# Kernel optimization log

Hardware: AMD Instinct MI355X
Metric: run time of the kernel (lower is better)

The kernel has to match this reference:

```python
import jax, jax.numpy as jnp
import numpy as np

C = 1.0          # curvature magnitude (args.c)
K = C            # geoopt Lorentz k parameter
EPS = 1e-15
NUM_LAYERS = 3   # resSumGCN propagation depth
CLAMP1 = 50.0    # dist2 clamp for id embeddings
CLAMP2 = 15.0    # dist2 clamp for tag embeddings

# ---- Lorentz manifold math (geoopt conventions, <x,x>_L = -K) ----

def projx(x):
    # project onto hyperboloid: x0 = sqrt(K + ||x_rest||^2)
    x0 = jnp.sqrt(K + jnp.sum(x[..., 1:] ** 2, axis=-1, keepdims=True))
    return jnp.concatenate([x0, x[..., 1:]], axis=-1)

def expmap0(u_rest):
    # exp map at origin; u_rest is the spatial part of the tangent vector
    sk = jnp.sqrt(K)
    norm = jnp.sqrt(jnp.clip(jnp.sum(u_rest ** 2, axis=-1, keepdims=True), EPS))
    x0 = sk * jnp.cosh(norm / sk)
    xr = sk * jnp.sinh(norm / sk) * u_rest / norm
    return jnp.concatenate([x0, xr], axis=-1)

def logmap0(x):
    # log map at origin; returns spatial part of tangent vector
    sk = jnp.sqrt(K)
    alpha = jnp.clip(x[..., :1] / sk, 1.0 + 1e-7)
    rest = x[..., 1:]
    rnorm = jnp.sqrt(jnp.clip(jnp.sum(rest ** 2, axis=-1, keepdims=True), EPS))
    return sk * jnp.arccosh(alpha) * rest / rnorm

def dist2(x, y):
    # squared geodesic distance, keepdim=True -> [..., 1]
    inner = -x[..., :1] * y[..., :1] + jnp.sum(x[..., 1:] * y[..., 1:], axis=-1, keepdims=True)
    d = jnp.clip(-inner / K, 1.0 + 1e-7)
    a = jnp.arccosh(d)
    return K * a * a

def l2p(x):
    # lorentz -> poincare: drops the time coordinate
    return x[..., 1:] / (x[..., :1] + jnp.sqrt(K))

def p2l(x):
    # poincare -> lorentz: adds the time coordinate
    nx = jnp.sum(x ** 2, axis=-1, keepdims=True)
    sk = jnp.sqrt(K)
    num = jnp.concatenate([K + nx, 2.0 * sk * x], axis=-1)
    return sk * num / (K - nx + 1e-6)

def p2k(x):
    denom = 1.0 + C * jnp.sum(x ** 2, axis=-1, keepdims=True)
    return 2.0 * x / denom

def k2p(x):
    denom = 1.0 + jnp.sqrt(jnp.clip(1.0 - C * jnp.sum(x ** 2, axis=-1, keepdims=True), EPS))
    return x / denom

def lorentz_factor(x):
    return 1.0 / jnp.sqrt(jnp.clip(1.0 - C * jnp.sum(x ** 2, axis=-1, keepdims=True), EPS))

def hyper_agg(weights, x):
    # Lorentz-factor weighted Einstein midpoint aggregation
    x_k = p2k(l2p(x))                                   # klein coords [T, d]
    gamma = lorentz_factor(jax.lax.stop_gradient(x_k))  # [T, 1] (detached)
    num = weights @ (gamma * x_k)                        # [M, d]
    den = jnp.clip(weights @ gamma, EPS)                 # [M, 1]
    return p2l(k2p(num / den))                           # [M, d+1]

def encoder_encode(x, edge_src, edge_dst, edge_weight, n_nodes):
    # HGCF-style resSumGCN: tangent-space propagation, sum of powers 1..L
    xt = logmap0(x)
    cur = xt
    acc = jnp.zeros_like(xt)
    for _ in range(NUM_LAYERS):
        msg = edge_weight[:, None] * cur[edge_src]       # [E, d]
        cur = jax.ops.segment_sum(msg, edge_dst, num_segments=n_nodes)
        acc = acc + cur
    return expmap0(acc)


def setup_inputs() -> dict:
    key = jax.random.key(0)
    ks = jax.random.split(key, 8)
    N_USERS, N_ITEMS, D, TAGS = 8192, 40960, 64, 1024
    N = N_USERS + N_ITEMS
    E, B = 1572864, 131072
    emb_weight = 0.1 * jax.random.normal(ks[0], (N, D), dtype=jnp.float32)
    T_weight = 0.1 * jax.random.normal(ks[1], (TAGS, D), dtype=jnp.float32)
    ugr_weight = 0.1 * jax.random.normal(ks[2], (N_USERS, D), dtype=jnp.float32)
    sps = jax.random.uniform(ks[3], (N_ITEMS, TAGS), dtype=jnp.float32)
    sps = sps / jnp.sum(sps, axis=1, keepdims=True)      # row-normalized tag matrix
    edge_src = jax.random.randint(ks[4], (E,), 0, N)
    edge_dst = jax.random.randint(ks[5], (E,), 0, N)
    edge_weight = jax.random.uniform(ks[6], (E,), dtype=jnp.float32) / 32.0
    u = jax.random.randint(ks[7], (B,), 0, N_USERS)
    i = jax.random.randint(jax.random.fold_in(key, 99), (B,), N_USERS, N)
    idx = jnp.stack([u, i], axis=1)
    return {"emb_weight": emb_weight, "T_weight": T_weight, "ugr_weight": ugr_weight,
            "sps": sps, "edge_weight": edge_weight, "edge_src": edge_src,
            "edge_dst": edge_dst, "idx": idx}


def reference(emb_weight, T_weight, ugr_weight, sps, edge_weight, edge_src, edge_dst, idx):
    N, D = emb_weight.shape
    # ---- encode ----
    x1 = projx(emb_weight)
    h_in = encoder_encode(x1, edge_src, edge_dst, edge_weight, N)   # [N, D]
    emb_tag = projx(T_weight)
    emb_tag_in = projx(ugr_weight)                                  # users
    emb_tag_out = hyper_agg(sps, emb_tag)                           # items [N_items, D]
    x2 = jnp.concatenate([emb_tag_in, emb_tag_out], axis=0)         # [N, D]
    h_gr = encoder_encode(x2, edge_src, edge_dst, edge_weight, N)   # [N, D]
    h = jnp.concatenate([h_in, h_gr], axis=-1)                      # [N, 2D]
    # ---- decode ----
    emb_in = h[idx[:, 0], :D]
    emb_out = h[idx[:, 1], :D]
    sq = jnp.minimum(dist2(emb_in, emb_out), CLAMP1)
    tag_in = h[idx[:, 0], D:]
    tag_out = h[idx[:, 1], D:]
    sq = sq + jnp.minimum(dist2(tag_in, tag_out), CLAMP2)
    return sq  # [B, 1]
```

## Files before the change

### kernel.cpp

```cpp
#include <hip/hip_runtime.h>


#define KSPLIT 2
#define NBUK 96
#define CAP 18432

__device__ __forceinline__ float wsum(float v) {
#pragma unroll
  for (int m = 32; m; m >>= 1) v += __shfl_xor(v, m, 64);
  return v;
}

__device__ __forceinline__ float logmap_scale(float ss) {
  float x0 = sqrtf(1.0f + ss);
  float alpha = fmaxf(x0, 1.0f + 1e-7f);
  float rnorm = sqrtf(fmaxf(ss, 1e-15f));
  return acoshf(alpha) / rnorm;
}


__device__ void passA_body(
    const int* __restrict__ esrc, const int* __restrict__ edst,
    const float* __restrict__ ew, int* __restrict__ bcur,
    int2* __restrict__ stage, int bx) {
  __shared__ int lh[128];
  __shared__ int lscan[128];
  __shared__ int lcur[128];
  __shared__ int gb[128];
  __shared__ unsigned int keyb[2048];
  __shared__ float wvb[2048];
  int tid = threadIdx.x;
  int base = bx * 2048;
  if (tid < 128) lh[tid] = 0;
  __syncthreads();
  unsigned int key[8]; float wv[8];
#pragma unroll
  for (int r = 0; r < 8; ++r) {
    int e = base + r * 256 + tid;
    int d = edst[e];
    key[r] = ((unsigned int)d << 16) | (unsigned int)esrc[e];
    wv[r] = ew[e];
    atomicAdd(&lh[d >> 9], 1);
  }
  __syncthreads();
  if (tid < 128) lscan[tid] = lh[tid];
  __syncthreads();
  for (int d = 1; d < 128; d <<= 1) {
    int v = (tid < 128 && tid >= d) ? lscan[tid - d] : 0;
    __syncthreads();
    if (tid < 128) lscan[tid] += v;
    __syncthreads();
  }
  if (tid < 128) {
    int excl = lscan[tid] - lh[tid];
    lscan[tid] = excl;
    lcur[tid] = 0;
    if (tid < NBUK && lh[tid] > 0) {
      int rsv = atomicAdd(&bcur[tid], lh[tid]);
      gb[tid] = tid * CAP + rsv;
    }
  }
  __syncthreads();
#pragma unroll
  for (int r = 0; r < 8; ++r) {
    int b = key[r] >> 25;
    int lp = lscan[b] + atomicAdd(&lcur[b], 1);
    keyb[lp] = key[r];
    wvb[lp] = wv[r];
  }
  __syncthreads();
#pragma unroll
  for (int r = 0; r < 8; ++r) {
    int i = r * 256 + tid;
    unsigned int k2 = keyb[i];
    int b = k2 >> 25;
    stage[gb[b] + (i - lscan[b])] = make_int2((int)k2, __float_as_int(wvb[i]));
  }
}

__device__ void prep_body(
    const float* __restrict__ emb, const float* __restrict__ ugr,
    const float* __restrict__ Tw, float* __restrict__ xt,
    float* __restrict__ gkg, int N, int NU, int TAGS, int pbx) {
  int n = pbx * 4 + (threadIdx.x >> 6);
  int lane = threadIdx.x & 63;
  if (n < N) {
    size_t base = (size_t)n * 128;
    float r1 = (lane < 63) ? emb[(size_t)n * 64 + 1 + lane] : 0.0f;
    float sc1 = logmap_scale(wsum(r1 * r1));
    if (lane < 63) xt[base + lane] = sc1 * r1;
    if (lane == 63) { xt[base + 126] = 0.0f; xt[base + 127] = 0.0f; }
    if (n < NU) {
      float r2 = (lane < 63) ? ugr[(size_t)n * 64 + 1 + lane] : 0.0f;
      float sc2 = logmap_scale(wsum(r2 * r2));
      if (lane < 63) xt[base + 63 + lane] = sc2 * r2;
    }
  } else if (n < N + TAGS) {
    int t = n - N;
    float r = (lane < 63) ? Tw[(size_t)t * 64 + 1 + lane] : 0.0f;
    float ss = wsum(r * r);
    float x0 = sqrtf(1.0f + ss);
    float p = r / (x0 + 1.0f);
    float sp = wsum(p * p);
    float k = 2.0f * p / (1.0f + sp);
    float sk2 = wsum(k * k);
    float gamma = 1.0f / sqrtf(fmaxf(1.0f - sk2, 1e-15f));
    gkg[(size_t)t * 64 + lane] = (lane < 63) ? gamma * k : gamma;
  }
}

__global__ __launch_bounds__(256) void k_mega1(
    const int* __restrict__ esrc, const int* __restrict__ edst,
    const float* __restrict__ ew, int* __restrict__ bcur,
    int2* __restrict__ stage,
    const float* __restrict__ emb, const float* __restrict__ ugr,
    const float* __restrict__ Tw, float* __restrict__ xt,
    float* __restrict__ gkg, int N, int NU, int TAGS, int nA) {
  if ((int)blockIdx.x < nA)
    passA_body(esrc, edst, ew, bcur, stage, blockIdx.x);
  else
    prep_body(emb, ugr, Tw, xt, gkg, N, NU, TAGS, blockIdx.x - nA);
}


__device__ void passB2_body(
    const int2* __restrict__ stage, const int* __restrict__ bcur,
    int* __restrict__ off, int2* __restrict__ rec, int N, int E) {
  __shared__ int hist[512];
  __shared__ int pairs[256];
  __shared__ int cur[512];
  __shared__ int bs[128];
  int b = blockIdx.x, tid = threadIdx.x;
  if (tid < 128) bs[tid] = (tid < NBUK) ? min(bcur[tid], CAP) : 0;
  hist[tid] = 0; hist[tid + 256] = 0;
  __syncthreads();
  for (int d = 1; d < 128; d <<= 1) {
    int v = (tid < 128 && tid >= d) ? bs[tid - d] : 0;
    __syncthreads();
    if (tid < 128) bs[tid] += v;
    __syncthreads();
  }
  int cnt = min(bcur[b], CAP);
  int base = bs[b] - cnt;
  if (b == 0 && tid == 0) off[N] = E;
  const int2* sg = stage + (size_t)b * CAP;
  for (int i = tid; i < cnt; i += 256)
    atomicAdd(&hist[((unsigned int)sg[i].x >> 16) & 511], 1);
  __syncthreads();
  int h0 = hist[2 * tid], h1 = hist[2 * tid + 1];
  int ps = h0 + h1;
  pairs[tid] = ps;
  __syncthreads();
  for (int d = 1; d < 256; d <<= 1) {
    int v = (tid >= d) ? pairs[tid - d] : 0;
    __syncthreads();
    pairs[tid] += v;
    __syncthreads();
  }
  int e0 = base + pairs[tid] - ps;
  int e1 = e0 + h0;
  int gd = b * 512 + 2 * tid;
  off[gd] = e0;      cur[2 * tid] = e0;
  off[gd + 1] = e1;  cur[2 * tid + 1] = e1;
  __syncthreads();
  for (int i = tid; i < cnt; i += 256) {
    int2 r = sg[i];
    unsigned int k2 = (unsigned int)r.x;
    int d = (int)((k2 >> 16) & 511);
    int p = atomicAdd(&cur[d], 1);
    rec[p] = make_int2((int)(k2 & 0xFFFF), r.y);
  }
}

__device__ void hyper_body(
    const float* __restrict__ sps, const float* __restrict__ gkg,
    float* __restrict__ pb, int NI, int bx, int ksp) {
  __shared__ float g_tile[32 * 64];
  int tid = threadIdx.x;
  int tx = tid & 15, ty = tid >> 4;
  int gx = tid & 15, gy = tid >> 4;
  int ib = bx * 64;
  int kbase = ksp * (1024 / KSPLIT);
  float acc[4][4];
#pragma unroll
  for (int c = 0; c < 4; ++c)
#pragma unroll
    for (int d = 0; d < 4; ++d) acc[c][d] = 0.0f;

  const float4* sps4 = (const float4*)sps;
  const float4* gkg4 = (const float4*)gkg;
  size_t rb[4];
#pragma unroll
  for (int c = 0; c < 4; ++c) rb[c] = (size_t)(ib + ty * 4 + c) * 256;

  for (int kc = 0; kc < (1024 / KSPLIT) / 32; ++kc) {
#pragma unroll
    for (int r = 0; r < 2; ++r) {
      int grow = gy + 16 * r;
      *(float4*)&g_tile[grow * 64 + gx * 4] =
          gkg4[(size_t)(kbase + kc * 32 + grow) * 16 + gx];
    }
    __syncthreads();
    int t4 = (kbase >> 2) + kc * 8;
    float4 A[4], Nb[4];
#pragma unroll
    for (int c = 0; c < 4; ++c) A[c] = sps4[rb[c] + t4];
#pragma unroll
    for (int tg = 0; tg < 8; ++tg) {
#pragma unroll
      for (int c = 0; c < 4; ++c)
        if (tg < 7) Nb[c] = sps4[rb[c] + t4 + tg + 1];
      float4 g4[4];
#pragma unroll
      for (int j = 0; j < 4; ++j)
        g4[j] = *(const float4*)&g_tile[(tg * 4 + j) * 64 + tx * 4];
#pragma unroll
      for (int c = 0; c < 4; ++c) {
        float sv[4] = {A[c].x, A[c].y, A[c].z, A[c].w};
#pragma unroll
        for (int j = 0; j < 4; ++j) {
          acc[c][0] = fmaf(sv[j], g4[j].x, acc[c][0]);
          acc[c][1] = fmaf(sv[j], g4[j].y, acc[c][1]);
          acc[c][2] = fmaf(sv[j], g4[j].z, acc[c][2]);
          acc[c][3] = fmaf(sv[j], g4[j].w, acc[c][3]);
        }
      }
#pragma unroll
      for (int c = 0; c < 4; ++c)
        if (tg < 7) A[c] = Nb[c];
    }
    __syncthreads();
  }

  float* dst = pb + ((size_t)ksp * NI + ib) * 64;
#pragma unroll
  for (int c = 0; c < 4; ++c)
    *(float4*)&dst[(size_t)(ty * 4 + c) * 64 + tx * 4] =
        make_float4(acc[c][0], acc[c][1], acc[c][2], acc[c][3]);
}

__global__ __launch_bounds__(256) void k_mega2(
    const int2* __restrict__ stage, const int* __restrict__ bcur,
    int* __restrict__ off, int2* __restrict__ rec,
    const float* __restrict__ sps, const float* __restrict__ gkg,
    float* __restrict__ pb, int NI, int N, int E) {
  if ((int)blockIdx.x < NBUK) {
    passB2_body(stage, bcur, off, rec, N, E);
  } else {
    int hb = blockIdx.x - NBUK;
    int nbx = NI / 64;
    hyper_body(sps, gkg, pb, NI, hb % nbx, hb / nbx);
  }
}

__global__ __launch_bounds__(256) void k_combine(
    const float* __restrict__ pb, float* __restrict__ xt, int NI, int NU) {
  int i = blockIdx.x * 4 + (threadIdx.x >> 6);
  if (i >= NI) return;
  int lane = threadIdx.x & 63;
  float v = 0.0f;
#pragma unroll
  for (int s = 0; s < KSPLIT; ++s) v += pb[((size_t)s * NI + i) * 64 + lane];
  float den = fmaxf(__shfl(v, 63, 64), 1e-15f);
  float y = v / den;
  float sy = wsum((lane < 63) ? y * y : 0.0f);
  float dk = 1.0f + sqrtf(fmaxf(1.0f - sy, 1e-15f));
  float q = y / dk;
  float nq = wsum((lane < 63) ? q * q : 0.0f);
  float f = 1.0f / (1.0f - nq + 1e-6f);
  float row0 = (1.0f + nq) * f;
  float r = 2.0f * q * f;
  float srr = wsum((lane < 63) ? r * r : 0.0f);
  float alpha = fmaxf(row0, 1.0f + 1e-7f);
  float scale = acoshf(alpha) / sqrtf(fmaxf(srr, 1e-15f));
  if (lane < 63)
    xt[(size_t)(NU + i) * 128 + 63 + lane] = scale * r;
}

__device__ __forceinline__ float4 gather_row(
    const float* __restrict__ cur, const int* __restrict__ off,
    const int2* __restrict__ rec, int n, int lane) {
  int half = lane >> 5;
  int q = lane & 31;
  const float4* cq = (const float4*)cur + q;
  int beg = off[n], end = off[n + 1];
  float4 acc = make_float4(0.0f, 0.0f, 0.0f, 0.0f);
  for (int j = beg; j < end; j += 64) {
    int cnt = min(64, end - j);
    int sv = 0; float wv = 0.0f;
    if (lane < cnt) {
      int2 rc = rec[j + lane];
      sv = rc.x;
      wv = __int_as_float(rc.y);
    }
    int k = 0;
    for (; k + 16 <= cnt; k += 16) {
      int s[8]; float w[8]; float4 v[8];
#pragma unroll
      for (int u = 0; u < 8; ++u) {
        int e = k + 2 * u + half;
        s[u] = __shfl(sv, e, 64);
        w[u] = __shfl(wv, e, 64);
      }
#pragma unroll
      for (int u = 0; u < 8; ++u) v[u] = cq[(size_t)s[u] * 32];
#pragma unroll
      for (int u = 0; u < 8; ++u) {
        acc.x = fmaf(w[u], v[u].x, acc.x);
        acc.y = fmaf(w[u], v[u].y, acc.y);
        acc.z = fmaf(w[u], v[u].z, acc.z);
        acc.w = fmaf(w[u], v[u].w, acc.w);
      }
    }
    for (; k + 8 <= cnt; k += 8) {
      int s[4]; float w[4]; float4 v[4];
#pragma unroll
      for (int u = 0; u < 4; ++u) {
        int e = k + 2 * u + half;
        s[u] = __shfl(sv, e, 64);
        w[u] = __shfl(wv, e, 64);
      }
#pragma unroll
      for (int u = 0; u < 4; ++u) v[u] = cq[(size_t)s[u] * 32];
#pragma unroll
      for (int u = 0; u < 4; ++u) {
        acc.x = fmaf(w[u], v[u].x, acc.x);
        acc.y = fmaf(w[u], v[u].y, acc.y);
        acc.z = fmaf(w[u], v[u].z, acc.z);
        acc.w = fmaf(w[u], v[u].w, acc.w);
      }
    }
    for (; k + 2 <= cnt; k += 2) {
      int e = k + half;
      int s0 = __shfl(sv, e, 64);
      float w0 = __shfl(wv, e, 64);
      float4 v = cq[(size_t)s0 * 32];
      acc.x = fmaf(w0, v.x, acc.x);
      acc.y = fmaf(w0, v.y, acc.y);
      acc.z = fmaf(w0, v.z, acc.z);
      acc.w = fmaf(w0, v.w, acc.w);
    }
    if (k < cnt) {
      int s0 = __shfl(sv, k, 64);
      float w0 = __shfl(wv, k, 64);
      if (half == 0) {
        float4 v = cq[(size_t)s0 * 32];
        acc.x = fmaf(w0, v.x, acc.x);
        acc.y = fmaf(w0, v.y, acc.y);
        acc.z = fmaf(w0, v.z, acc.z);
        acc.w = fmaf(w0, v.w, acc.w);
      }
    }
  }
  acc.x += __shfl_xor(acc.x, 32, 64);
  acc.y += __shfl_xor(acc.y, 32, 64);
  acc.z += __shfl_xor(acc.z, 32, 64);
  acc.w += __shfl_xor(acc.w, 32, 64);
  return acc;
}

__global__ __launch_bounds__(256) void k_gather(
    const float* __restrict__ cur, float* __restrict__ nxt,
    const int* __restrict__ off, const int2* __restrict__ rec, int N) {
  int n = blockIdx.x * 4 + (threadIdx.x >> 6);
  if (n >= N) return;
  int lane = threadIdx.x & 63;
  float4 acc = gather_row(cur, off, rec, n, lane);
  if (lane < 32) ((float4*)(nxt + (size_t)n * 128))[lane] = acc;
}

__global__ __launch_bounds__(256) void k_gather_exp(
    const float* __restrict__ cur, const float* b1, const float* __restrict__ b2,
    const int* __restrict__ off, const int2* __restrict__ rec,
    float* h, int N) {
  int n = blockIdx.x * 4 + (threadIdx.x >> 6);
  if (n >= N) return;
  int lane = threadIdx.x & 63;
  int q = lane & 31;
  float4 a3 = gather_row(cur, off, rec, n, lane);
  size_t b = (size_t)n * 128;
  float4 r1 = ((const float4*)(b1 + b))[q];
  float4 r2 = ((const float4*)(b2 + b))[q];
  float vv[4] = {a3.x + r1.x + r2.x, a3.y + r1.y + r2.y,
                 a3.z + r1.z + r2.z, a3.w + r1.w + r2.w};
  float p0 = 0.0f, p1 = 0.0f;
#pragma unroll
  for (int i = 0; i < 4; ++i) {
    int c = 4 * q + i;
    if (c < 63) p0 += vv[i] * vv[i]; else p1 += vv[i] * vv[i];
  }
  float ss0 = 0.5f * wsum(p0);
  float ss1 = 0.5f * wsum(p1);
  float nn0 = sqrtf(fmaxf(ss0, 1e-15f)), nn1 = sqrtf(fmaxf(ss1, 1e-15f));
  float s0 = sinhf(nn0) / nn0, s1 = sinhf(nn1) / nn1;
  int prev = (lane == 0) ? 0 : lane - 1;
  float pv2 = __shfl(vv[2], prev, 64);
  float pv3 = __shfl(vv[3], prev, 64);
  if (lane < 32) {
    float4 o;
    if (q < 16) {
      o.x = (q == 0) ? coshf(nn0) : s0 * pv3;
      o.y = s0 * vv[0]; o.z = s0 * vv[1]; o.w = s0 * vv[2];
    } else {
      o.x = (q == 16) ? coshf(nn1) : s1 * pv2;
      o.y = s1 * pv3; o.z = s1 * vv[0]; o.w = s1 * vv[1];
    }
    ((float4*)(h + b))[q] = o;
  }
}

__global__ __launch_bounds__(256) void k_score(
    const float* __restrict__ h, const int* __restrict__ idx,
    float* __restrict__ out, int B) {
  int w = blockIdx.x * 4 + (threadIdx.x >> 6);
  int lane = threadIdx.x & 63;
  int b0 = w * 4;
  if (b0 >= B) return;
  int np = min(4, B - b0);
  float2 hu[4], hv[4];
#pragma unroll
  for (int p = 0; p < 4; ++p) {
    int bb = b0 + ((p < np) ? p : 0);
    int u = idx[2 * bb], v = idx[2 * bb + 1];
    hu[p] = ((const float2*)(h + (size_t)u * 128))[lane];
    hv[p] = ((const float2*)(h + (size_t)v * 128))[lane];
  }
#pragma unroll
  for (int p = 0; p < 4; ++p) {
    if (p >= np) break;
    float px = hu[p].x * hv[p].x;
    if (lane == 0 || lane == 32) px = -px;
    float pp = px + hu[p].y * hv[p].y;
#pragma unroll
    for (int m = 1; m < 32; m <<= 1) pp += __shfl_xor(pp, m, 64);
    float dd = fmaxf(-pp, 1.0f + 1e-7f);
    float a = acoshf(dd);
    float s = fminf(a * a, (lane < 32) ? 50.0f : 15.0f);
    s += __shfl_xor(s, 32, 64);
    if (lane == 0) out[b0 + p] = s;
  }
}

extern "C" void kernel_launch(void* const* d_in, const int* in_sizes, int n_in,
                              void* d_out, int out_size, void* d_ws, size_t ws_size,
                              hipStream_t stream) {
  const float* emb = (const float*)d_in[0];
  const float* Tw  = (const float*)d_in[1];
  const float* ugr = (const float*)d_in[2];
  const float* sps = (const float*)d_in[3];
  const float* ew  = (const float*)d_in[4];
  const int* esrc  = (const int*)d_in[5];
  const int* edst  = (const int*)d_in[6];
  const int* idx   = (const int*)d_in[7];
  float* out = (float*)d_out;

  const int N    = in_sizes[0] / 64;
  const int TAGS = in_sizes[1] / 64;
  const int NU   = in_sizes[2] / 64;
  const int NI   = in_sizes[3] / TAGS;
  const int E    = in_sizes[4];
  const int B    = in_sizes[7] / 2;

  size_t rowsz = (size_t)N * 128 * sizeof(float);
  char* ws = (char*)d_ws;
  float* xt  = (float*)(ws);
  float* b1  = (float*)(ws + rowsz);
  float* b2  = (float*)(ws + 2 * rowsz);
  float* gkg = (float*)(ws + 3 * rowsz);
  size_t o = 3 * rowsz + (size_t)TAGS * 64 * sizeof(float);
  int* off   = (int*)(ws + o);  o += (size_t)(N + 1) * sizeof(int);
  int* bcur  = (int*)(ws + o);  o += (size_t)NBUK * sizeof(int);
  o = (o + 7) & ~(size_t)7;
  int2* rec = (int2*)(ws + o);
  int2* stage = (int2*)b2;
  float* pb = b1;
  float* h  = b1;

  const int nA = E / 2048;
  const int nPrep = (N + TAGS + 3) / 4;
  const int nHyper = (NI / 64) * KSPLIT;

  hipMemsetAsync(bcur, 0, (size_t)NBUK * sizeof(int), stream);
  k_mega1<<<nA + nPrep, 256, 0, stream>>>(esrc, edst, ew, bcur, stage,
                                          emb, ugr, Tw, xt, gkg, N, NU, TAGS, nA);
  k_mega2<<<NBUK + nHyper, 256, 0, stream>>>(stage, bcur, off, rec,
                                             sps, gkg, pb, NI, N, E);
  k_combine<<<(NI + 3) / 4, 256, 0, stream>>>(pb, xt, NI, NU);

  k_gather<<<(N + 3) / 4, 256, 0, stream>>>(xt, b1, off, rec, N);
  k_gather<<<(N + 3) / 4, 256, 0, stream>>>(b1, b2, off, rec, N);
  k_gather_exp<<<(N + 3) / 4, 256, 0, stream>>>(b2, b1, b2, off, rec, h, N);

  k_score<<<(B / 4 + 3) / 4, 256, 0, stream>>>(h, idx, out, B);
}
```

Baseline: 545.2 us.

## Split fused pass-B/hyper kernel and retile hyper GEMM with shared-memory sps tile

Splits the combined bucket-sort pass and hyperbolic aggregation GEMM back into two separate kernel launches. The GEMM now stages a 128x32 tile of the sparse-weight matrix in padded shared memory, where before each thread streamed its rows straight from global memory. Each thread computes an 8x4 output block instead of 4x4, and KSPLIT goes from 2 to 4, with the grid laid out as a 2D (rows, k-split) grid. The aim is better reuse and coalescing of sps loads, at the cost of losing overlap between the two passes and doing more partial-sum work in combine.

```diff
diff --git a/kernel.cpp b/kernel.cpp
--- a/kernel.cpp
+++ b/kernel.cpp
@@ -1,7 +1,7 @@
 #include <hip/hip_runtime.h>
 
 
-#define KSPLIT 2
+#define KSPLIT 4
 #define NBUK 96
 #define CAP 18432
 
@@ -123,7 +123,7 @@
 }
 
 
-__device__ void passB2_body(
+__global__ __launch_bounds__(256) void k_passB2(
     const int2* __restrict__ stage, const int* __restrict__ bcur,
     int* __restrict__ off, int2* __restrict__ rec, int N, int E) {
   __shared__ int hist[512];
@@ -172,51 +172,50 @@
   }
 }
 
-__device__ void hyper_body(
+__global__ __launch_bounds__(256) void k_hyper(
     const float* __restrict__ sps, const float* __restrict__ gkg,
-    float* __restrict__ pb, int NI, int bx, int ksp) {
-  __shared__ float g_tile[32 * 64];
+    float* __restrict__ pb, int NI) {
+  __shared__ float s_tile[128][36];
+  __shared__ float g_tile[32][64];
   int tid = threadIdx.x;
   int tx = tid & 15, ty = tid >> 4;
+  int sx = tid & 7,  sy = tid >> 3;
   int gx = tid & 15, gy = tid >> 4;
-  int ib = bx * 64;
-  int kbase = ksp * (1024 / KSPLIT);
-  float acc[4][4];
-#pragma unroll
-  for (int c = 0; c < 4; ++c)
+  int ib = blockIdx.x * 128;
+  int kbase = blockIdx.y * 256;
+  float acc[8][4];
+#pragma unroll
+  for (int c = 0; c < 8; ++c)
 #pragma unroll
     for (int d = 0; d < 4; ++d) acc[c][d] = 0.0f;
 
   const float4* sps4 = (const float4*)sps;
   const float4* gkg4 = (const float4*)gkg;
-  size_t rb[4];
-#pragma unroll
-  for (int c = 0; c < 4; ++c) rb[c] = (size_t)(ib + ty * 4 + c) * 256;
-
-  for (int kc = 0; kc < (1024 / KSPLIT) / 32; ++kc) {
+
+  for (int kc = 0; kc < 8; ++kc) {
+    int t4b = (kbase >> 2) + kc * 8;
+#pragma unroll
+    for (int r = 0; r < 4; ++r) {
+      int row = sy + 32 * r;
+      *(float4*)&s_tile[row][sx * 4] = sps4[(size_t)(ib + row) * 256 + t4b + sx];
+    }
 #pragma unroll
     for (int r = 0; r < 2; ++r) {
       int grow = gy + 16 * r;
-      *(float4*)&g_tile[grow * 64 + gx * 4] =
+      *(float4*)&g_tile[grow][gx * 4] =
           gkg4[(size_t)(kbase + kc * 32 + grow) * 16 + gx];
     }
     __syncthreads();
-    int t4 = (kbase >> 2) + kc * 8;
-    float4 A[4], Nb[4];
-#pragma unroll
-    for (int c = 0; c < 4; ++c) A[c] = sps4[rb[c] + t4];
 #pragma unroll
     for (int tg = 0; tg < 8; ++tg) {
-#pragma unroll
-      for (int c = 0; c < 4; ++c)
-        if (tg < 7) Nb[c] = sps4[rb[c] + t4 + tg + 1];
       float4 g4[4];
 #pragma unroll
       for (int j = 0; j < 4; ++j)
-        g4[j] = *(const float4*)&g_tile[(tg * 4 + j) * 64 + tx * 4];
-#pragma unroll
-      for (int c = 0; c < 4; ++c) {
-        float sv[4] = {A[c].x, A[c].y, A[c].z, A[c].w};
+        g4[j] = *(const float4*)&g_tile[tg * 4 + j][tx * 4];
+#pragma unroll
+      for (int c = 0; c < 8; ++c) {
+        float4 s4 = *(const float4*)&s_tile[ty + 16 * c][tg * 4];
+        float sv[4] = {s4.x, s4.y, s4.z, s4.w};
 #pragma unroll
         for (int j = 0; j < 4; ++j) {
           acc[c][0] = fmaf(sv[j], g4[j].x, acc[c][0]);
@@ -225,32 +224,15 @@
           acc[c][3] = fmaf(sv[j], g4[j].w, acc[c][3]);
         }
       }
-#pragma unroll
-      for (int c = 0; c < 4; ++c)
-        if (tg < 7) A[c] = Nb[c];
-    }
-    __syncthreads();
-  }
-
-  float* dst = pb + ((size_t)ksp * NI + ib) * 64;
-#pragma unroll
-  for (int c = 0; c < 4; ++c)
-    *(float4*)&dst[(size_t)(ty * 4 + c) * 64 + tx * 4] =
+    }
+    __syncthreads();
+  }
+
+  float* dst = pb + ((size_t)blockIdx.y * NI + ib) * 64;
+#pragma unroll
+  for (int c = 0; c < 8; ++c)
+    *(float4*)&dst[(size_t)(ty + 16 * c) * 64 + tx * 4] =
         make_float4(acc[c][0], acc[c][1], acc[c][2], acc[c][3]);
-}
-
-__global__ __launch_bounds__(256) void k_mega2(
-    const int2* __restrict__ stage, const int* __restrict__ bcur,
-    int* __restrict__ off, int2* __restrict__ rec,
-    const float* __restrict__ sps, const float* __restrict__ gkg,
-    float* __restrict__ pb, int NI, int N, int E) {
-  if ((int)blockIdx.x < NBUK) {
-    passB2_body(stage, bcur, off, rec, N, E);
-  } else {
-    int hb = blockIdx.x - NBUK;
-    int nbx = NI / 64;
-    hyper_body(sps, gkg, pb, NI, hb % nbx, hb / nbx);
-  }
 }
 
 __global__ __launch_bounds__(256) void k_combine(
@@ -478,13 +460,13 @@
 
   const int nA = E / 2048;
   const int nPrep = (N + TAGS + 3) / 4;
-  const int nHyper = (NI / 64) * KSPLIT;
 
   hipMemsetAsync(bcur, 0, (size_t)NBUK * sizeof(int), stream);
   k_mega1<<<nA + nPrep, 256, 0, stream>>>(esrc, edst, ew, bcur, stage,
                                           emb, ugr, Tw, xt, gkg, N, NU, TAGS, nA);
-  k_mega2<<<NBUK + nHyper, 256, 0, stream>>>(stage, bcur, off, rec,
-                                             sps, gkg, pb, NI, N, E);
+  k_passB2<<<NBUK, 256, 0, stream>>>(stage, bcur, off, rec, N, E);
+  dim3 hgrid(NI / 128, KSPLIT);
+  k_hyper<<<hgrid, 256, 0, stream>>>(sps, gkg, pb, NI);
   k_combine<<<(NI + 3) / 4, 256, 0, stream>>>(pb, xt, NI, NU);
 
   k_gather<<<(N + 3) / 4, 256, 0, stream>>>(xt, b1, off, rec, N);
```

Result: no change. 539.4 us (-1.1%).
